# Kernel optimization log

Measured on AMD Instinct MI355X. Metric: run time of the kernel, lower is better.

## Reference

```python
import jax, jax.numpy as jnp
import numpy as np

CHUNK = 512
LR = 0.001  # fast-weight learning_rate


def setup_inputs() -> dict:
    key = jax.random.key(0)
    k1, k2, k3, k4 = jax.random.split(key, 4)
    B, S, H, F = 4, 4096, 1024, 4096
    x = jax.random.normal(k1, (B, S, H), dtype=jnp.float32)
    w0 = jax.random.normal(k2, (H, F), dtype=jnp.float32) * 0.02
    w1 = jax.random.normal(k3, (F, H), dtype=jnp.float32) * 0.02
    w2 = jax.random.normal(k4, (H, F), dtype=jnp.float32) * 0.02
    return {"x": x, "w0": w0, "w1": w1, "w2": w2}


def _fast_weight(xc, a0, a1, a2):
    # SwiGLU fast-weight MLP (LaCT-style): [B,C,H] -> [B,C,H]
    h = jax.nn.silu(jnp.einsum('bch,hf->bcf', xc, a0)) * jnp.einsum('bch,hf->bcf', xc, a2)
    return jnp.einsum('bcf,fh->bch', h, a1)


def reference(x, w0, w1, w2):
    B, S, H = x.shape
    nC = S // CHUNK
    # [nC, B, CHUNK, H] so scan iterates over chunks
    xc = x.reshape(B, nC, CHUNK, H).transpose(1, 0, 2, 3)

    def step(carry, x_chunk):
        a0, a1, a2, acc_loss = carry
        out = _fast_weight(x_chunk, a0, a1, a2)
        chunk_loss = jnp.mean((out - x_chunk) ** 2)
        decay = 1.0 - LR * chunk_loss  # per-chunk scalar weight decay
        return (a0 * decay, a1 * decay, a2 * decay, acc_loss + chunk_loss), out

    init = (w0, w1, w2, jnp.float32(0.0))
    (_, _, _, total_loss), outs = jax.lax.scan(step, init, xc)
    output = outs.transpose(1, 0, 2, 3).reshape(B, S, H)
    return output, total_loss / nC
```

## Files before the change

### kernel.cpp

```cpp
#include <hip/hip_runtime.h>

typedef float f32x4 __attribute__((ext_vector_type(4)));
typedef short bf16x8 __attribute__((ext_vector_type(8)));
typedef unsigned short u16;

#define B_SZ 4
#define S_SZ 4096
#define H_SZ 1024
#define F_SZ 4096
#define CHUNK_SZ 512
#define NCHUNK 8
#define MCH 2048
#define LRATE 0.001f
#define NSPLIT 4

__device__ __forceinline__ u16 f2bf(float f) {
  unsigned u = __float_as_uint(f);
  u += 0x7FFFu + ((u >> 16) & 1u);
  return (u16)(u >> 16);
}
__device__ __forceinline__ float bf2f(u16 u) {
  return __uint_as_float(((unsigned)u) << 16);
}

__device__ __forceinline__ void gload_lds16(const void* g, void* l) {
  __builtin_amdgcn_global_load_lds(
      (const __attribute__((address_space(1))) unsigned int*)g,
      (__attribute__((address_space(3))) unsigned int*)l, 16, 0, 0);
}


__global__ __launch_bounds__(256) void k_init(float* scal) {
  if (threadIdx.x == 0) { scal[0] = 1.f; scal[1] = 0.f; }
}

__global__ __launch_bounds__(256) void k_cvt_x(const float* __restrict__ x,
                                               u16* __restrict__ xb) {
  size_t i = ((size_t)blockIdx.x * 256 + threadIdx.x) * 8;
  float4 v0 = *(const float4*)(x + i);
  float4 v1 = *(const float4*)(x + i + 4);
  union { u16 u[8]; bf16x8 v; } o;
  o.u[0] = f2bf(v0.x); o.u[1] = f2bf(v0.y); o.u[2] = f2bf(v0.z); o.u[3] = f2bf(v0.w);
  o.u[4] = f2bf(v1.x); o.u[5] = f2bf(v1.y); o.u[6] = f2bf(v1.z); o.u[7] = f2bf(v1.w);
  *(bf16x8*)(xb + i) = o.v;
}

__global__ __launch_bounds__(256) void k_transpose_cvt(const float* __restrict__ W,
                                                       u16* __restrict__ Wt,
                                                       int R, int C) {
  __shared__ float tile[32][33];
  int tx = threadIdx.x & 31, ty = threadIdx.x >> 5;
  int r0 = blockIdx.y << 5, c0 = blockIdx.x << 5;
#pragma unroll
  for (int i = 0; i < 4; i++)
    tile[ty + i * 8][tx] = W[(size_t)(r0 + ty + i * 8) * C + c0 + tx];
  __syncthreads();
#pragma unroll
  for (int i = 0; i < 4; i++)
    Wt[(size_t)(c0 + ty + i * 8) * R + r0 + tx] = f2bf(tile[tx][ty + i * 8]);
}

__global__ __launch_bounds__(256, 2) void k_gemm_gu(
    const u16* __restrict__ xb,
    const u16* __restrict__ w0t,
    const u16* __restrict__ w2t,
    u16* __restrict__ hbuf,
    const float* __restrict__ scal, int chunk) {
  __shared__ __align__(16) u16 sA[128 * 64];
  __shared__ __align__(16) u16 sB0[128 * 64];
  __shared__ __align__(16) u16 sB2[128 * 64];

  int t = threadIdx.x;
  int lane = t & 63, wid = t >> 6;
  int wm = wid >> 1, wn = wid & 1;

  int orig = blockIdx.x + (gridDim.x * blockIdx.y);
  int nwg = gridDim.x * gridDim.y;
  int wg = (orig & 7) * (nwg >> 3) + (orig >> 3);
  int tm = wg & 15, tn = wg >> 4;

  int gm0 = tm << 7;
  int bb = gm0 >> 9;
  int pos0 = gm0 & 511;
  const u16* Abase = xb + ((size_t)bb * S_SZ + (size_t)chunk * CHUNK_SZ + pos0) * H_SZ;

  int srow = t >> 3;
  int scol = (((t & 7) ^ (srow & 7)) << 3);
  const u16* aSrc  = Abase + (size_t)srow * H_SZ + scol;
  const u16* b0Src = w0t + ((size_t)(tn << 7) + srow) * H_SZ + scol;
  const u16* b2Src = w2t + ((size_t)(tn << 7) + srow) * H_SZ + scol;
  char* aDst  = (char*)sA  + t * 16;
  char* b0Dst = (char*)sB0 + t * 16;
  char* b2Dst = (char*)sB2 + t * 16;

  f32x4 acc0[4][4], acc2[4][4];
#pragma unroll
  for (int i = 0; i < 4; i++)
#pragma unroll
    for (int j = 0; j < 4; j++)
#pragma unroll
      for (int k = 0; k < 4; k++) { acc0[i][j][k] = 0.f; acc2[i][j][k] = 0.f; }

  int arow = (wm << 6) + (lane & 15);
  int brow = (wn << 6) + (lane & 15);
  int sl0 = (lane >> 4) ^ (lane & 7);
  int sl1 = ((lane >> 4) | 4) ^ (lane & 7);
  const int aO0 = arow * 128 + sl0 * 16, aO1 = arow * 128 + sl1 * 16;
  const int bO0 = brow * 128 + sl0 * 16, bO1 = brow * 128 + sl1 * 16;

#pragma unroll 1
  for (int k0 = 0; k0 < H_SZ; k0 += 64) {
#pragma unroll
    for (int r = 0; r < 4; r++) {
      gload_lds16(aSrc  + (size_t)r * 32 * H_SZ, aDst  + r * 4096);
      gload_lds16(b0Src + (size_t)r * 32 * H_SZ, b0Dst + r * 4096);
      gload_lds16(b2Src + (size_t)r * 32 * H_SZ, b2Dst + r * 4096);
    }
    aSrc += 64; b0Src += 64; b2Src += 64;
    __syncthreads();

    {
      bf16x8 av[4], b0v[4], b2v[4];
#pragma unroll
      for (int fr = 0; fr < 4; fr++) av[fr] = *(const bf16x8*)((const char*)sA + aO0 + fr * 2048);
#pragma unroll
      for (int fc = 0; fc < 4; fc++) {
        b0v[fc] = *(const bf16x8*)((const char*)sB0 + bO0 + fc * 2048);
        b2v[fc] = *(const bf16x8*)((const char*)sB2 + bO0 + fc * 2048);
      }
#pragma unroll
      for (int fr = 0; fr < 4; fr++)
#pragma unroll
        for (int fc = 0; fc < 4; fc++) {
          acc0[fr][fc] = __builtin_amdgcn_mfma_f32_16x16x32_bf16(av[fr], b0v[fc], acc0[fr][fc], 0, 0, 0);
          acc2[fr][fc] = __builtin_amdgcn_mfma_f32_16x16x32_bf16(av[fr], b2v[fc], acc2[fr][fc], 0, 0, 0);
        }
    }
    {
      bf16x8 av[4], b0v[4], b2v[4];
#pragma unroll
      for (int fr = 0; fr < 4; fr++) av[fr] = *(const bf16x8*)((const char*)sA + aO1 + fr * 2048);
#pragma unroll
      for (int fc = 0; fc < 4; fc++) {
        b0v[fc] = *(const bf16x8*)((const char*)sB0 + bO1 + fc * 2048);
        b2v[fc] = *(const bf16x8*)((const char*)sB2 + bO1 + fc * 2048);
      }
#pragma unroll
      for (int fr = 0; fr < 4; fr++)
#pragma unroll
        for (int fc = 0; fc < 4; fc++) {
          acc0[fr][fc] = __builtin_amdgcn_mfma_f32_16x16x32_bf16(av[fr], b0v[fc], acc0[fr][fc], 0, 0, 0);
          acc2[fr][fc] = __builtin_amdgcn_mfma_f32_16x16x32_bf16(av[fr], b2v[fc], acc2[fr][fc], 0, 0, 0);
        }
    }
    __syncthreads();
  }

  float D = scal[0];
#pragma unroll
  for (int fr = 0; fr < 4; fr++)
#pragma unroll
    for (int fc = 0; fc < 4; fc++) {
      int row0 = (tm << 7) + (wm << 6) + (fr << 4) + ((lane >> 4) << 2);
      int col = (tn << 7) + (wn << 6) + (fc << 4) + (lane & 15);
#pragma unroll
      for (int j = 0; j < 4; j++) {
        float g = D * acc0[fr][fc][j];
        float u = D * acc2[fr][fc][j];
        float sil = g / (1.f + __expf(-g));
        hbuf[(size_t)(row0 + j) * F_SZ + col] = f2bf(sil * u);
      }
    }
}

__global__ __launch_bounds__(256) void k_gemm_out(
    const u16* __restrict__ hbuf,
    const u16* __restrict__ w1t,
    u16* __restrict__ pbuf) {
  __shared__ __align__(16) u16 sA[128 * 64];
  __shared__ __align__(16) u16 sB[64 * 64];

  int t = threadIdx.x;
  int lane = t & 63, wid = t >> 6;
  int wm = wid >> 1, wn = wid & 1;
  int tm = blockIdx.x, tn = blockIdx.y, kz = blockIdx.z;

  int srow = t >> 3;
  int scol = (((t & 7) ^ (srow & 7)) << 3);
  const u16* aSrc = hbuf + ((size_t)(tm << 7) + srow) * F_SZ + kz * 1024 + scol;
  const u16* bSrc = w1t + ((size_t)(tn << 6) + srow) * F_SZ + kz * 1024 + scol;
  char* aDst = (char*)sA + t * 16;
  char* bDst = (char*)sB + t * 16;

  f32x4 acc[4][2];
#pragma unroll
  for (int i = 0; i < 4; i++)
#pragma unroll
    for (int j = 0; j < 2; j++)
#pragma unroll
      for (int k = 0; k < 4; k++) acc[i][j][k] = 0.f;

  int arow = (wm << 6) + (lane & 15);
  int brow = (wn << 5) + (lane & 15);
  int sl0 = (lane >> 4) ^ (lane & 7);
  int sl1 = ((lane >> 4) | 4) ^ (lane & 7);
  const int aO0 = arow * 128 + sl0 * 16, aO1 = arow * 128 + sl1 * 16;
  const int bO0 = brow * 128 + sl0 * 16, bO1 = brow * 128 + sl1 * 16;

#pragma unroll 1
  for (int k0 = 0; k0 < 1024; k0 += 64) {
#pragma unroll
    for (int r = 0; r < 4; r++)
      gload_lds16(aSrc + (size_t)r * 32 * F_SZ, aDst + r * 4096);
#pragma unroll
    for (int r = 0; r < 2; r++)
      gload_lds16(bSrc + (size_t)r * 32 * F_SZ, bDst + r * 4096);
    aSrc += 64; bSrc += 64;
    __syncthreads();

    {
      bf16x8 av[4], bv[2];
#pragma unroll
      for (int fr = 0; fr < 4; fr++) av[fr] = *(const bf16x8*)((const char*)sA + aO0 + fr * 2048);
#pragma unroll
      for (int fc = 0; fc < 2; fc++) bv[fc] = *(const bf16x8*)((const char*)sB + bO0 + fc * 2048);
#pragma unroll
      for (int fr = 0; fr < 4; fr++)
#pragma unroll
        for (int fc = 0; fc < 2; fc++)
          acc[fr][fc] = __builtin_amdgcn_mfma_f32_16x16x32_bf16(av[fr], bv[fc], acc[fr][fc], 0, 0, 0);
    }
    {
      bf16x8 av[4], bv[2];
#pragma unroll
      for (int fr = 0; fr < 4; fr++) av[fr] = *(const bf16x8*)((const char*)sA + aO1 + fr * 2048);
#pragma unroll
      for (int fc = 0; fc < 2; fc++) bv[fc] = *(const bf16x8*)((const char*)sB + bO1 + fc * 2048);
#pragma unroll
      for (int fr = 0; fr < 4; fr++)
#pragma unroll
        for (int fc = 0; fc < 2; fc++)
          acc[fr][fc] = __builtin_amdgcn_mfma_f32_16x16x32_bf16(av[fr], bv[fc], acc[fr][fc], 0, 0, 0);
    }
    __syncthreads();
  }

#pragma unroll
  for (int fr = 0; fr < 4; fr++)
#pragma unroll
    for (int fc = 0; fc < 2; fc++) {
      int row0 = (tm << 7) + (wm << 6) + (fr << 4) + ((lane >> 4) << 2);
      int col = (tn << 6) + (wn << 5) + (fc << 4) + (lane & 15);
#pragma unroll
      for (int j = 0; j < 4; j++)
        pbuf[((size_t)kz * MCH + row0 + j) * 1024 + col] = f2bf(acc[fr][fc][j]);
    }
}

__global__ __launch_bounds__(256) void k_epilogue(
    const u16* __restrict__ pbuf, const float* __restrict__ x,
    float* __restrict__ out, const float* __restrict__ scal,
    float* __restrict__ partials, int chunk) {
  __shared__ float red[256];
  int t = threadIdx.x;
  size_t base = ((size_t)blockIdx.x * 256 + t) * 8;
  int row = (int)(base >> 10);
  int col = (int)(base & 1023);
  float D = scal[0];

  float s[8] = {0.f, 0.f, 0.f, 0.f, 0.f, 0.f, 0.f, 0.f};
#pragma unroll
  for (int kz = 0; kz < NSPLIT; kz++) {
    union { bf16x8 v; u16 u[8]; } p;
    p.v = *(const bf16x8*)(pbuf + (size_t)kz * MCH * 1024 + base);
#pragma unroll
    for (int j = 0; j < 8; j++) s[j] += bf2f(p.u[j]);
  }

  int bb = row >> 9, pos = row & 511;
  size_t off = ((size_t)bb * S_SZ + (size_t)chunk * CHUNK_SZ + pos) * H_SZ + col;
  float4 x0 = *(const float4*)(x + off);
  float4 x1 = *(const float4*)(x + off + 4);
  float xv[8] = {x0.x, x0.y, x0.z, x0.w, x1.x, x1.y, x1.z, x1.w};
  float ov[8];
  float psum = 0.f;
#pragma unroll
  for (int j = 0; j < 8; j++) {
    ov[j] = D * s[j];
    float e = ov[j] - xv[j];
    psum += e * e;
  }
  *(float4*)(out + off) = make_float4(ov[0], ov[1], ov[2], ov[3]);
  *(float4*)(out + off + 4) = make_float4(ov[4], ov[5], ov[6], ov[7]);

  red[t] = psum;
  __syncthreads();
  for (int s2 = 128; s2 > 0; s2 >>= 1) {
    if (t < s2) red[t] += red[t + s2];
    __syncthreads();
  }
  if (t == 0) partials[blockIdx.x] = red[0];
}

__global__ __launch_bounds__(256) void k_update(float* scal, const float* __restrict__ partials,
                                                float* lossout, int chunk) {
  __shared__ float red[256];
  int t = threadIdx.x;
  float s = 0.f;
  for (int i = t; i < 1024; i += 256) s += partials[i];
  red[t] = s;
  __syncthreads();
  for (int s2 = 128; s2 > 0; s2 >>= 1) {
    if (t < s2) red[t] += red[t + s2];
    __syncthreads();
  }
  if (t == 0) {
    float loss = red[0] / (float)((size_t)MCH * H_SZ);
    float total = scal[1] + loss;
    scal[1] = total;
    scal[0] = scal[0] * (1.f - LRATE * loss);
    if (chunk == NCHUNK - 1) lossout[0] = total / (float)NCHUNK;
  }
}

extern "C" void kernel_launch(void* const* d_in, const int* in_sizes, int n_in,
                              void* d_out, int out_size, void* d_ws, size_t ws_size,
                              hipStream_t stream) {
  const float* x = (const float*)d_in[0];
  const float* w0 = (const float*)d_in[1];
  const float* w1 = (const float*)d_in[2];
  const float* w2 = (const float*)d_in[3];
  float* out = (float*)d_out;

  char* ws = (char*)d_ws;
  float* scal = (float*)ws;
  float* partials = (float*)(ws + 1024);
  u16* xb = (u16*)(ws + 8192);
  u16* w0t = xb + (size_t)B_SZ * S_SZ * H_SZ;
  u16* w2t = w0t + (size_t)H_SZ * F_SZ;
  u16* w1t = w2t + (size_t)H_SZ * F_SZ;
  u16* hbuf = w1t + (size_t)F_SZ * H_SZ;
  u16* pbuf = hbuf + (size_t)MCH * F_SZ;

  k_init<<<1, 256, 0, stream>>>(scal);
  k_cvt_x<<<(B_SZ * S_SZ * H_SZ) / (256 * 8), 256, 0, stream>>>(x, xb);
  k_transpose_cvt<<<dim3(F_SZ / 32, H_SZ / 32), 256, 0, stream>>>(w0, w0t, H_SZ, F_SZ);
  k_transpose_cvt<<<dim3(H_SZ / 32, F_SZ / 32), 256, 0, stream>>>(w1, w1t, F_SZ, H_SZ);
  k_transpose_cvt<<<dim3(F_SZ / 32, H_SZ / 32), 256, 0, stream>>>(w2, w2t, H_SZ, F_SZ);

  float* lossout = out + (size_t)B_SZ * S_SZ * H_SZ;
  for (int c = 0; c < NCHUNK; c++) {
    k_gemm_gu<<<dim3(16, 32), 256, 0, stream>>>(xb, w0t, w2t, hbuf, scal, c);
    k_gemm_out<<<dim3(16, 16, NSPLIT), 256, 0, stream>>>(hbuf, w1t, pbuf);
    k_epilogue<<<1024, 256, 0, stream>>>(pbuf, x, out, scal, partials, c);
    k_update<<<1, 256, 0, stream>>>(scal, partials, lossout, c);
  }
}
```

Before: 606.4 us.

## Interleave gate/up weights into one 256x256 double-buffered GEMM and fuse loss update

Interleaves the transposed w0 and w2 rows so the gate and up projections become a single GEMM with a 256x256 tile. The new kernel uses 512 threads, double-buffered LDS prefetch and MFMA priority hints. The SwiGLU epilogue pairs the gate and up values across adjacent lanes with a shuffle. The separate loss-update kernel is folded into the epilogue through a last-block atomic counter, removing one launch per chunk. The larger tile uses 128KB of LDS and many accumulator registers, which may limit occupancy.

```diff
diff --git a/kernel.cpp b/kernel.cpp
--- a/kernel.cpp
+++ b/kernel.cpp
@@ -29,9 +29,13 @@
       (__attribute__((address_space(3))) unsigned int*)l, 16, 0, 0);
 }
 
-
-__global__ __launch_bounds__(256) void k_init(float* scal) {
-  if (threadIdx.x == 0) { scal[0] = 1.f; scal[1] = 0.f; }
+#define VMCNT0() asm volatile("s_waitcnt vmcnt(0)" ::: "memory")
+#define SBAR() __builtin_amdgcn_s_barrier()
+#define SCHED_FENCE() __builtin_amdgcn_sched_barrier(0)
+
+
+__global__ __launch_bounds__(256) void k_init(float* scal, int* cnt) {
+  if (threadIdx.x == 0) { scal[0] = 1.f; scal[1] = 0.f; cnt[0] = 0; }
 }
 
 __global__ __launch_bounds__(256) void k_cvt_x(const float* __restrict__ x,
@@ -47,7 +51,7 @@
 
 __global__ __launch_bounds__(256) void k_transpose_cvt(const float* __restrict__ W,
                                                        u16* __restrict__ Wt,
-                                                       int R, int C) {
+                                                       int R, int C, int rstride, int roff) {
   __shared__ float tile[32][33];
   int tx = threadIdx.x & 31, ty = threadIdx.x >> 5;
   int r0 = blockIdx.y << 5, c0 = blockIdx.x << 5;
@@ -57,118 +61,122 @@
   __syncthreads();
 #pragma unroll
   for (int i = 0; i < 4; i++)
-    Wt[(size_t)(c0 + ty + i * 8) * R + r0 + tx] = f2bf(tile[tx][ty + i * 8]);
-}
-
-__global__ __launch_bounds__(256, 2) void k_gemm_gu(
+    Wt[((size_t)(c0 + ty + i * 8) * rstride + roff) * R + r0 + tx] = f2bf(tile[tx][ty + i * 8]);
+}
+
+__global__ __launch_bounds__(512, 2) void k_gemm_gu8(
     const u16* __restrict__ xb,
-    const u16* __restrict__ w0t,
-    const u16* __restrict__ w2t,
+    const u16* __restrict__ wgu,
     u16* __restrict__ hbuf,
     const float* __restrict__ scal, int chunk) {
-  __shared__ __align__(16) u16 sA[128 * 64];
-  __shared__ __align__(16) u16 sB0[128 * 64];
-  __shared__ __align__(16) u16 sB2[128 * 64];
+  __shared__ __align__(16) u16 sA[2][256 * 64];
+  __shared__ __align__(16) u16 sB[2][256 * 64];
 
   int t = threadIdx.x;
   int lane = t & 63, wid = t >> 6;
-  int wm = wid >> 1, wn = wid & 1;
-
-  int orig = blockIdx.x + (gridDim.x * blockIdx.y);
-  int nwg = gridDim.x * gridDim.y;
-  int wg = (orig & 7) * (nwg >> 3) + (orig >> 3);
-  int tm = wg & 15, tn = wg >> 4;
-
-  int gm0 = tm << 7;
+  int wm = wid >> 2, wn = wid & 3;
+
+  int orig = blockIdx.x;
+  int wg = (orig & 7) * 32 + (orig >> 3);
+  int tn = wg >> 3, tm = wg & 7;
+
+  int gm0 = tm << 8;
   int bb = gm0 >> 9;
   int pos0 = gm0 & 511;
   const u16* Abase = xb + ((size_t)bb * S_SZ + (size_t)chunk * CHUNK_SZ + pos0) * H_SZ;
 
-  int srow = t >> 3;
-  int scol = (((t & 7) ^ (srow & 7)) << 3);
-  const u16* aSrc  = Abase + (size_t)srow * H_SZ + scol;
-  const u16* b0Src = w0t + ((size_t)(tn << 7) + srow) * H_SZ + scol;
-  const u16* b2Src = w2t + ((size_t)(tn << 7) + srow) * H_SZ + scol;
-  char* aDst  = (char*)sA  + t * 16;
-  char* b0Dst = (char*)sB0 + t * 16;
-  char* b2Dst = (char*)sB2 + t * 16;
-
-  f32x4 acc0[4][4], acc2[4][4];
-#pragma unroll
-  for (int i = 0; i < 4; i++)
+  int scol = (((t & 7) ^ ((t >> 3) & 7)) << 3);
+  const u16* aS = Abase + (size_t)(t >> 3) * H_SZ + scol;
+  const u16* bS = wgu + ((size_t)(tn << 8) + (t >> 3)) * H_SZ + scol;
+
+  f32x4 acc[8][4];
+#pragma unroll
+  for (int i = 0; i < 8; i++)
 #pragma unroll
     for (int j = 0; j < 4; j++)
 #pragma unroll
-      for (int k = 0; k < 4; k++) { acc0[i][j][k] = 0.f; acc2[i][j][k] = 0.f; }
-
-  int arow = (wm << 6) + (lane & 15);
-  int brow = (wn << 6) + (lane & 15);
-  int sl0 = (lane >> 4) ^ (lane & 7);
-  int sl1 = ((lane >> 4) | 4) ^ (lane & 7);
-  const int aO0 = arow * 128 + sl0 * 16, aO1 = arow * 128 + sl1 * 16;
-  const int bO0 = brow * 128 + sl0 * 16, bO1 = brow * 128 + sl1 * 16;
+      for (int k = 0; k < 4; k++) acc[i][j][k] = 0.f;
+
+  const int aBase0 = ((wm << 7) + (lane & 15)) * 128;
+  const int bBase0 = ((wn << 6) + (lane & 15)) * 128;
+  const int sb0 = (((lane >> 4)) ^ (lane & 7)) * 16;
+  const int sb1 = (((lane >> 4) | 4) ^ (lane & 7)) * 16;
+
+#define GA(sb_, kt_, s_) gload_lds16(aS + (size_t)(s_) * 64 * H_SZ + (kt_) * 64, \
+                                     (char*)sA + (sb_) * 32768 + (s_) * 8192 + t * 16)
+#define GB(sb_, kt_, s_) gload_lds16(bS + (size_t)(s_) * 64 * H_SZ + (kt_) * 64, \
+                                     (char*)sB + (sb_) * 32768 + (s_) * 8192 + t * 16)
+
+#define GU8_QUAD(cbo, FRS, FCS)                                            \
+  {                                                                        \
+    const char* aB = (const char*)sA + (cbo);                              \
+    const char* bB = (const char*)sB + (cbo);                              \
+    bf16x8 av[4][2], bv[2][2];                                             \
+    _Pragma("unroll")                                                      \
+    for (int i = 0; i < 4; i++) {                                          \
+      av[i][0] = *(const bf16x8*)(aB + aBase0 + (FRS + i) * 2048 + sb0);   \
+      av[i][1] = *(const bf16x8*)(aB + aBase0 + (FRS + i) * 2048 + sb1);   \
+    }                                                                      \
+    _Pragma("unroll")                                                      \
+    for (int j = 0; j < 2; j++) {                                          \
+      bv[j][0] = *(const bf16x8*)(bB + bBase0 + (FCS + j) * 2048 + sb0);   \
+      bv[j][1] = *(const bf16x8*)(bB + bBase0 + (FCS + j) * 2048 + sb1);   \
+    }                                                                      \
+    SBAR();                                                                \
+    __builtin_amdgcn_s_setprio(1);                                         \
+    _Pragma("unroll")                                                      \
+    for (int i = 0; i < 4; i++)                                            \
+      _Pragma("unroll")                                                    \
+      for (int j = 0; j < 2; j++) {                                        \
+        acc[FRS + i][FCS + j] = __builtin_amdgcn_mfma_f32_16x16x32_bf16(   \
+            av[i][0], bv[j][0], acc[FRS + i][FCS + j], 0, 0, 0);           \
+        acc[FRS + i][FCS + j] = __builtin_amdgcn_mfma_f32_16x16x32_bf16(   \
+            av[i][1], bv[j][1], acc[FRS + i][FCS + j], 0, 0, 0);           \
+      }                                                                    \
+    __builtin_amdgcn_s_setprio(0);                                         \
+  }
+
+  GA(0, 0, 0); GA(0, 0, 1); GA(0, 0, 2); GA(0, 0, 3);
+  GB(0, 0, 0); GB(0, 0, 1); GB(0, 0, 2); GB(0, 0, 3);
+  VMCNT0();
+  SBAR();
 
 #pragma unroll 1
-  for (int k0 = 0; k0 < H_SZ; k0 += 64) {
-#pragma unroll
-    for (int r = 0; r < 4; r++) {
-      gload_lds16(aSrc  + (size_t)r * 32 * H_SZ, aDst  + r * 4096);
-      gload_lds16(b0Src + (size_t)r * 32 * H_SZ, b0Dst + r * 4096);
-      gload_lds16(b2Src + (size_t)r * 32 * H_SZ, b2Dst + r * 4096);
-    }
-    aSrc += 64; b0Src += 64; b2Src += 64;
-    __syncthreads();
-
-    {
-      bf16x8 av[4], b0v[4], b2v[4];
-#pragma unroll
-      for (int fr = 0; fr < 4; fr++) av[fr] = *(const bf16x8*)((const char*)sA + aO0 + fr * 2048);
-#pragma unroll
-      for (int fc = 0; fc < 4; fc++) {
-        b0v[fc] = *(const bf16x8*)((const char*)sB0 + bO0 + fc * 2048);
-        b2v[fc] = *(const bf16x8*)((const char*)sB2 + bO0 + fc * 2048);
-      }
-#pragma unroll
-      for (int fr = 0; fr < 4; fr++)
-#pragma unroll
-        for (int fc = 0; fc < 4; fc++) {
-          acc0[fr][fc] = __builtin_amdgcn_mfma_f32_16x16x32_bf16(av[fr], b0v[fc], acc0[fr][fc], 0, 0, 0);
-          acc2[fr][fc] = __builtin_amdgcn_mfma_f32_16x16x32_bf16(av[fr], b2v[fc], acc2[fr][fc], 0, 0, 0);
-        }
-    }
-    {
-      bf16x8 av[4], b0v[4], b2v[4];
-#pragma unroll
-      for (int fr = 0; fr < 4; fr++) av[fr] = *(const bf16x8*)((const char*)sA + aO1 + fr * 2048);
-#pragma unroll
-      for (int fc = 0; fc < 4; fc++) {
-        b0v[fc] = *(const bf16x8*)((const char*)sB0 + bO1 + fc * 2048);
-        b2v[fc] = *(const bf16x8*)((const char*)sB2 + bO1 + fc * 2048);
-      }
-#pragma unroll
-      for (int fr = 0; fr < 4; fr++)
-#pragma unroll
-        for (int fc = 0; fc < 4; fc++) {
-          acc0[fr][fc] = __builtin_amdgcn_mfma_f32_16x16x32_bf16(av[fr], b0v[fc], acc0[fr][fc], 0, 0, 0);
-          acc2[fr][fc] = __builtin_amdgcn_mfma_f32_16x16x32_bf16(av[fr], b2v[fc], acc2[fr][fc], 0, 0, 0);
-        }
-    }
-    __syncthreads();
+  for (int kt = 0; kt < 16; kt++) {
+    int cb = kt & 1, nb = cb ^ 1;
+    int cbo = cb * 32768;
+    bool st = (kt < 15);
+    if (st) { GA(nb, kt + 1, 0); GA(nb, kt + 1, 1); }
+    GU8_QUAD(cbo, 0, 0);
+    SBAR(); SCHED_FENCE();
+    if (st) { GA(nb, kt + 1, 2); GA(nb, kt + 1, 3); }
+    GU8_QUAD(cbo, 0, 2);
+    SBAR(); SCHED_FENCE();
+    if (st) { GB(nb, kt + 1, 0); GB(nb, kt + 1, 1); }
+    GU8_QUAD(cbo, 4, 0);
+    SBAR(); SCHED_FENCE();
+    if (st) { GB(nb, kt + 1, 2); GB(nb, kt + 1, 3); }
+    GU8_QUAD(cbo, 4, 2);
+    if (st) VMCNT0();
+    SBAR(); SCHED_FENCE();
   }
 
   float D = scal[0];
 #pragma unroll
-  for (int fr = 0; fr < 4; fr++)
+  for (int fr = 0; fr < 8; fr++)
 #pragma unroll
     for (int fc = 0; fc < 4; fc++) {
-      int row0 = (tm << 7) + (wm << 6) + (fr << 4) + ((lane >> 4) << 2);
-      int col = (tn << 7) + (wn << 6) + (fc << 4) + (lane & 15);
+      int row0 = (tm << 8) + (wm << 7) + (fr << 4) + ((lane >> 4) << 2);
+      int col = (tn << 8) + (wn << 6) + (fc << 4) + (lane & 15);
+      int f = col >> 1;
 #pragma unroll
       for (int j = 0; j < 4; j++) {
-        float g = D * acc0[fr][fc][j];
-        float u = D * acc2[fr][fc][j];
-        float sil = g / (1.f + __expf(-g));
-        hbuf[(size_t)(row0 + j) * F_SZ + col] = f2bf(sil * u);
+        float v = acc[fr][fc][j];
+        float w = __shfl_xor(v, 1);
+        float g = D * ((lane & 1) ? w : v);
+        float u = D * ((lane & 1) ? v : w);
+        float h = (g / (1.f + __expf(-g))) * u;
+        if (!(lane & 1)) hbuf[(size_t)(row0 + j) * F_SZ + f] = f2bf(h);
       }
     }
 }
@@ -259,9 +267,10 @@
 
 __global__ __launch_bounds__(256) void k_epilogue(
     const u16* __restrict__ pbuf, const float* __restrict__ x,
-    float* __restrict__ out, const float* __restrict__ scal,
-    float* __restrict__ partials, int chunk) {
+    float* __restrict__ out, float* scal,
+    float* partials, int* cnt, float* lossout, int chunk) {
   __shared__ float red[256];
+  __shared__ int amLast;
   int t = threadIdx.x;
   size_t base = ((size_t)blockIdx.x * 256 + t) * 8;
   int row = (int)(base >> 10);
@@ -299,27 +308,30 @@
     if (t < s2) red[t] += red[t + s2];
     __syncthreads();
   }
-  if (t == 0) partials[blockIdx.x] = red[0];
-}
-
-__global__ __launch_bounds__(256) void k_update(float* scal, const float* __restrict__ partials,
-                                                float* lossout, int chunk) {
-  __shared__ float red[256];
-  int t = threadIdx.x;
-  float s = 0.f;
-  for (int i = t; i < 1024; i += 256) s += partials[i];
-  red[t] = s;
+  if (t == 0) {
+    __hip_atomic_store(&partials[blockIdx.x], red[0], __ATOMIC_RELEASE, __HIP_MEMORY_SCOPE_AGENT);
+    int old = __hip_atomic_fetch_add(cnt, 1, __ATOMIC_ACQ_REL, __HIP_MEMORY_SCOPE_AGENT);
+    amLast = (old == 1023);
+  }
   __syncthreads();
-  for (int s2 = 128; s2 > 0; s2 >>= 1) {
-    if (t < s2) red[t] += red[t + s2];
+  if (amLast) {
+    float ps = 0.f;
+    for (int i = t; i < 1024; i += 256)
+      ps += __hip_atomic_load(&partials[i], __ATOMIC_ACQUIRE, __HIP_MEMORY_SCOPE_AGENT);
+    red[t] = ps;
     __syncthreads();
-  }
-  if (t == 0) {
-    float loss = red[0] / (float)((size_t)MCH * H_SZ);
-    float total = scal[1] + loss;
-    scal[1] = total;
-    scal[0] = scal[0] * (1.f - LRATE * loss);
-    if (chunk == NCHUNK - 1) lossout[0] = total / (float)NCHUNK;
+    for (int s2 = 128; s2 > 0; s2 >>= 1) {
+      if (t < s2) red[t] += red[t + s2];
+      __syncthreads();
+    }
+    if (t == 0) {
+      float loss = red[0] / (float)((size_t)MCH * H_SZ);
+      float total = scal[1] + loss;
+      scal[1] = total;
+      scal[0] = scal[0] * (1.f - LRATE * loss);
+      if (chunk == NCHUNK - 1) lossout[0] = total / (float)NCHUNK;
+      __hip_atomic_store(cnt, 0, __ATOMIC_RELEASE, __HIP_MEMORY_SCOPE_AGENT);
+    }
   }
 }
 
@@ -334,25 +346,25 @@
 
   char* ws = (char*)d_ws;
   float* scal = (float*)ws;
+  int* cnt = (int*)(ws + 512);
   float* partials = (float*)(ws + 1024);
   u16* xb = (u16*)(ws + 8192);
-  u16* w0t = xb + (size_t)B_SZ * S_SZ * H_SZ;
-  u16* w2t = w0t + (size_t)H_SZ * F_SZ;
-  u16* w1t = w2t + (size_t)H_SZ * F_SZ;
+  u16* wgu = xb + (size_t)B_SZ * S_SZ * H_SZ;
+  u16* w1t = wgu + (size_t)2 * H_SZ * F_SZ / 1;
+  w1t = wgu + (size_t)8192 * 1024;
   u16* hbuf = w1t + (size_t)F_SZ * H_SZ;
   u16* pbuf = hbuf + (size_t)MCH * F_SZ;
 
-  k_init<<<1, 256, 0, stream>>>(scal);
+  k_init<<<1, 256, 0, stream>>>(scal, cnt);
   k_cvt_x<<<(B_SZ * S_SZ * H_SZ) / (256 * 8), 256, 0, stream>>>(x, xb);
-  k_transpose_cvt<<<dim3(F_SZ / 32, H_SZ / 32), 256, 0, stream>>>(w0, w0t, H_SZ, F_SZ);
-  k_transpose_cvt<<<dim3(H_SZ / 32, F_SZ / 32), 256, 0, stream>>>(w1, w1t, F_SZ, H_SZ);
-  k_transpose_cvt<<<dim3(F_SZ / 32, H_SZ / 32), 256, 0, stream>>>(w2, w2t, H_SZ, F_SZ);
+  k_transpose_cvt<<<dim3(F_SZ / 32, H_SZ / 32), 256, 0, stream>>>(w0, wgu, H_SZ, F_SZ, 2, 0);
+  k_transpose_cvt<<<dim3(F_SZ / 32, H_SZ / 32), 256, 0, stream>>>(w2, wgu, H_SZ, F_SZ, 2, 1);
+  k_transpose_cvt<<<dim3(H_SZ / 32, F_SZ / 32), 256, 0, stream>>>(w1, w1t, F_SZ, H_SZ, 1, 0);
 
   float* lossout = out + (size_t)B_SZ * S_SZ * H_SZ;
   for (int c = 0; c < NCHUNK; c++) {
-    k_gemm_gu<<<dim3(16, 32), 256, 0, stream>>>(xb, w0t, w2t, hbuf, scal, c);
+    k_gemm_gu8<<<dim3(256), 512, 0, stream>>>(xb, wgu, hbuf, scal, c);
     k_gemm_out<<<dim3(16, 16, NSPLIT), 256, 0, stream>>>(hbuf, w1t, pbuf);
-    k_epilogue<<<1024, 256, 0, stream>>>(pbuf, x, out, scal, partials, c);
-    k_update<<<1, 256, 0, stream>>>(scal, partials, lossout, c);
-  }
-}
+    k_epilogue<<<1024, 256, 0, stream>>>(pbuf, x, out, scal, partials, cnt, lossout, c);
+  }
+}
```

Result: slower. 1.326 ms (+118.6%).
